# Kernel tuning notes

Hardware: AMD Instinct MI355X
Metric: run time of the kernel (lower is better)

The kernel has to match this reference:

```python
import jax, jax.numpy as jnp
import numpy as np

B, N, T, DM, H, M = 32, 207, 24, 64, 8, 32
E = 2 * DM  # true input feature dim (2*dmodel per the reshape in the source)


def setup_inputs() -> dict:
    rng = jax.random.key(0)
    ks = jax.random.split(rng, 10)
    s = 0.05  # scale params to keep activations numerically sane
    query = jax.random.normal(ks[0], (B, N, T, E), jnp.float32)
    key = jax.random.normal(ks[1], (B, N, T, E), jnp.float32)
    value = jax.random.normal(ks[2], (B, N, T, E), jnp.float32)
    # causal temporal mask, broadcast over batch/node/head; True = masked out
    atten_mask = jnp.broadcast_to(jnp.triu(jnp.ones((T, T), bool), 1), (B, N, 1, T, T))
    qp1 = jax.random.normal(ks[3], (N * DM, M), jnp.float32) * s
    qp2 = jax.random.normal(ks[4], (M, 4 * DM), jnp.float32) * s
    kp1 = jax.random.normal(ks[5], (N * DM, M), jnp.float32) * s
    kp2 = jax.random.normal(ks[6], (M, 4 * DM), jnp.float32) * s
    vp1 = jax.random.normal(ks[7], (N * DM, M), jnp.float32) * s
    vp2 = jax.random.normal(ks[8], (M, 4 * DM), jnp.float32) * s
    out_W = jax.random.normal(ks[9], (E, DM), jnp.float32) * s
    out_b = jnp.zeros((DM,), jnp.float32)
    return dict(query=query, key=key, value=value, atten_mask=atten_mask,
                qp1=qp1, qp2=qp2, kp1=kp1, kp2=kp2, vp1=vp1, vp2=vp2,
                out_W=out_W, out_b=out_b, num_heads=H)


def reference(query, key, value, atten_mask, qp1, qp2, kp1, kp2, vp1, vp2, out_W, out_b, num_heads):
    b, n, t, e = query.shape

    def proj(x, p1, p2):
        # low-rank factored per-node projection: (N*dmodel, M) @ (M, 4*dmodel) -> (N, E, E)
        P = (p1 @ p2).reshape(n, e, e)
        y = jnp.einsum('bnti,nik->bntk', x, P)
        return jax.nn.relu(y).reshape(b, n, t, num_heads, -1)

    q = proj(query, qp1, qp2)   # (B,N,T,H,d)
    k = proj(key, kp1, kp2)
    v = proj(value, vp1, vp2)

    scale = 1.0 / np.sqrt(q.shape[-1]).astype(np.float32)
    scores = jnp.einsum('bnthe,bnshe->bnhts', q, k)          # (B,N,H,T,S)
    scores = jnp.where(atten_mask, -jnp.inf, scores)          # masked_fill before scaling
    attn = jax.nn.softmax(scale * scores, axis=-1)            # dropout disabled (eval)
    out = jnp.einsum('bnhts,bnshd->bnthd', attn, v).reshape(b, n, t, -1)
    out = jax.nn.relu(out @ out_W + out_b)                    # (B,N,T,dmodel)
    return out, attn
```

## Files before the change

### kernel.cpp

```cpp
#include <hip/hip_runtime.h>
#include <hip/hip_bf16.h>

#define Bn 32
#define Nn 207
#define Tt 24
#define Ee 128
#define Hh 8
#define Dm 64
#define Mm 32
#define NBN (Bn * Nn)
#define PT ((size_t)Nn * 16384)

typedef __attribute__((ext_vector_type(8))) short bf16x8;
typedef __attribute__((ext_vector_type(4))) float f32x4;

__device__ __forceinline__ unsigned swz256(unsigned a) { return a ^ (((a >> 8) & 7u) << 4); }
__device__ __forceinline__ unsigned swz64(unsigned a)  { return a ^ (((a >> 7) & 3u) << 4); }
__device__ __forceinline__ unsigned cvtpk(float lo, float hi) {
  unsigned r;
  asm("v_cvt_pk_bf16_f32 %0, %1, %2" : "=v"(r) : "v"(lo), "v"(hi));
  return r;
}
__device__ __forceinline__ unsigned short f2bs(float f) {
  return (unsigned short)cvtpk(f, f);
}

__global__ __launch_bounds__(256) void build_P_frag3(
    const float* __restrict__ qp1, const float* __restrict__ qp2,
    const float* __restrict__ kp1, const float* __restrict__ kp2,
    const float* __restrict__ vp1, const float* __restrict__ vp2,
    unsigned short* __restrict__ Pt) {
  const int tau = blockIdx.y;
  const float* p1 = (tau == 0) ? qp1 : (tau == 1) ? kp1 : vp1;
  const float* p2 = (tau == 0) ? qp2 : (tau == 1) ? kp2 : vp2;
  unsigned short* dst = Pt + (size_t)tau * PT;
  const int bid = blockIdx.x;
  const int n = bid >> 3;
  const int r8 = bid & 7;
  const int ks = r8 >> 1;
  const int chunk = ((r8 & 1) << 1) + (threadIdx.x >> 7);
  const int col = threadIdx.x & 127;
  const int base_i = ks * 32 + chunk * 8;
  const float* p1r = p1 + (size_t)(n * 64 + (base_i >> 1)) * Mm;
  const float* p2a = p2 + col;
  const float* p2b = p2 + 128 + col;
  float acc[8] = {};
#pragma unroll
  for (int m = 0; m < Mm; ++m) {
    float a = p2a[m * 256], b = p2b[m * 256];
#pragma unroll
    for (int jj = 0; jj < 4; ++jj) {
      float pv = p1r[jj * Mm + m];
      acc[2 * jj]     = fmaf(pv, a, acc[2 * jj]);
      acc[2 * jj + 1] = fmaf(pv, b, acc[2 * jj + 1]);
    }
  }
  const int nt = col >> 4;
  const int lane = (chunk << 4) | (col & 15);
  union { unsigned u[4]; uint4 v; } w;
#pragma unroll
  for (int jj = 0; jj < 4; ++jj) w.u[jj] = cvtpk(acc[2 * jj], acc[2 * jj + 1]);
  *(uint4*)(dst + (size_t)(((n * 8 + nt) * 4 + ks) * 64 + lane) * 8) = w.v;
}

__global__ __launch_bounds__(256) void build_W_frag(const float* __restrict__ W,
                                                    unsigned short* __restrict__ Wt) {
  for (int idx = threadIdx.x; idx < 1024; idx += 256) {
    int lane = idx & 63, ks = (idx >> 6) & 3, nt = idx >> 8;
    union { unsigned u[4]; uint4 v; } w;
#pragma unroll
    for (int jj = 0; jj < 4; ++jj) {
      float a = W[(size_t)(ks * 32 + (lane >> 4) * 8 + 2 * jj) * 64 + nt * 16 + (lane & 15)];
      float b = W[(size_t)(ks * 32 + (lane >> 4) * 8 + 2 * jj + 1) * 64 + nt * 16 + (lane & 15)];
      w.u[jj] = cvtpk(a, b);
    }
    *(uint4*)(Wt + (size_t)idx * 8) = w.v;
  }
}

__global__ __launch_bounds__(256, 4) void fused_attn(
    const float* __restrict__ Qin, const float* __restrict__ Kin,
    const float* __restrict__ Vin,
    const unsigned short* __restrict__ Ptq, const unsigned short* __restrict__ Ptk,
    const unsigned short* __restrict__ Ptv, const unsigned short* __restrict__ Wt,
    const float* __restrict__ bias,
    float* __restrict__ out, float* __restrict__ attn) {
  __shared__ __align__(16) char smem[38912];
  const int tid = threadIdx.x;
  const int lane = tid & 63;
  const int wv = tid >> 6;
  const int c = lane & 15;
  const int g = lane >> 4;
  const f32x4 zf = {0.f, 0.f, 0.f, 0.f};
  const bf16x8 zb = {0, 0, 0, 0, 0, 0, 0, 0};

  int bx = blockIdx.x;
  bx = (bx & 7) * 828 + (bx >> 3);
  const int n = bx >> 5;
  const int b = bx & 31;
  const size_t xbase = (size_t)(b * Nn + n) * (Tt * Ee);

  {
    uint4 z4 = {0, 0, 0, 0};
    *(uint4*)(smem + 30720 + tid * 32) = z4;
    *(uint4*)(smem + 30720 + tid * 32 + 16) = z4;
    const float* src[3] = {Qin + xbase, Kin + xbase, Vin + xbase};
#pragma unroll
    for (int w = 0; w < 3; ++w)
#pragma unroll
      for (int it = 0; it < 3; ++it) {
        int e4 = tid + 256 * it;
        float4 xv = *(const float4*)(src[w] + (size_t)e4 * 4);
        unsigned a = swz256((unsigned)((e4 >> 5) * 256 + (e4 & 31) * 8));
        uint2 pk;
        pk.x = cvtpk(xv.x, xv.y);
        pk.y = cvtpk(xv.z, xv.w);
        *(uint2*)(smem + w * 6144 + a) = pk;
      }
  }
  __syncthreads();

  {
#pragma unroll
    for (int w = 0; w < 3; ++w) {
      const unsigned short* Pf = (w == 0) ? Ptq : (w == 1) ? Ptk : Ptv;
      f32x4 acc[2][2] = {{zf, zf}, {zf, zf}};
#pragma unroll
      for (int ks = 0; ks < 4; ++ks) {
        bf16x8 Bf[2], Af[2];
#pragma unroll
        for (int ntl = 0; ntl < 2; ++ntl)
          Bf[ntl] = *(const bf16x8*)(Pf + (size_t)(((n * 8 + (wv * 2 + ntl)) * 4 + ks) * 64 + lane) * 8);
#pragma unroll
        for (int mt = 0; mt < 2; ++mt) {
          int row = mt * 16 + c; row = row < 24 ? row : 23;
          Af[mt] = *(const bf16x8*)(smem + w * 6144 + swz256((unsigned)(row * 256 + ks * 64 + g * 16)));
        }
        __builtin_amdgcn_s_setprio(1);
#pragma unroll
        for (int mt = 0; mt < 2; ++mt)
#pragma unroll
          for (int ntl = 0; ntl < 2; ++ntl)
            acc[mt][ntl] = __builtin_amdgcn_mfma_f32_16x16x32_bf16(Af[mt], Bf[ntl], acc[mt][ntl], 0, 0, 0);
        __builtin_amdgcn_s_setprio(0);
      }
      if (w < 2) {
        const float postscale = (w == 0) ? 0.25f : 1.0f;
        char* dst = smem + 18432 + w * 6144;
#pragma unroll
        for (int mt = 0; mt < 2; ++mt)
#pragma unroll
          for (int r = 0; r < 4; ++r) {
            int row = mt * 16 + g * 4 + r;
            if (row < 24) {
#pragma unroll
              for (int ntl = 0; ntl < 2; ++ntl) {
                int col = (wv * 2 + ntl) * 16 + c;
                *(unsigned short*)(dst + swz256((unsigned)(row * 256 + col * 2))) =
                    f2bs(fmaxf(acc[mt][ntl][r], 0.f) * postscale);
              }
            }
          }
      } else {
#pragma unroll
        for (int mt = 0; mt < 2; ++mt)
#pragma unroll
          for (int r = 0; r < 4; ++r) {
            int srow = mt * 16 + g * 4 + r;
            if (srow < 24) {
#pragma unroll
              for (int ntl = 0; ntl < 2; ++ntl) {
                int dcol = (wv * 2 + ntl) * 16 + c;
                *(unsigned short*)(smem + 30720 + swz64((unsigned)(dcol * 64 + srow * 2))) =
                    f2bs(fmaxf(acc[mt][ntl][r], 0.f));
              }
            }
          }
      }
    }
  }
  __syncthreads();

  {
    const size_t abase = (size_t)(b * Nn + n) * (Hh * Tt * Tt);
#pragma unroll
    for (int hh = 0; hh < 2; ++hh) {
      int h = wv * 2 + hh;
      bf16x8 Aq[2], Bk[2];
#pragma unroll
      for (int mt = 0; mt < 2; ++mt) {
        int row = mt * 16 + c; row = row < 24 ? row : 23;
        Aq[mt] = zb;
        if (lane < 32) Aq[mt] = *(const bf16x8*)(smem + 18432 + swz256((unsigned)(row * 256 + (h * 16 + g * 8) * 2)));
      }
#pragma unroll
      for (int st = 0; st < 2; ++st) {
        int row = st * 16 + c; row = row < 24 ? row : 23;
        Bk[st] = zb;
        if (lane < 32) Bk[st] = *(const bf16x8*)(smem + 24576 + swz256((unsigned)(row * 256 + (h * 16 + g * 8) * 2)));
      }
      f32x4 sc[2][2];
      __builtin_amdgcn_s_setprio(1);
#pragma unroll
      for (int mt = 0; mt < 2; ++mt)
#pragma unroll
        for (int st = 0; st < 2; ++st)
          sc[mt][st] = __builtin_amdgcn_mfma_f32_16x16x32_bf16(Aq[mt], Bk[st], zf, 0, 0, 0);
      __builtin_amdgcn_s_setprio(0);
#pragma unroll
      for (int mt = 0; mt < 2; ++mt)
#pragma unroll
        for (int r = 0; r < 4; ++r) {
          int t = mt * 16 + g * 4 + r;
          float e0 = (c <= t)      ? __expf(sc[mt][0][r]) : 0.f;
          float e1 = (16 + c <= t) ? __expf(sc[mt][1][r]) : 0.f;
          float s2 = e0 + e1;
          s2 += __shfl_xor(s2, 1);
          s2 += __shfl_xor(s2, 2);
          s2 += __shfl_xor(s2, 4);
          s2 += __shfl_xor(s2, 8);
          float inv = 1.0f / s2;
          float p0 = e0 * inv, p1 = e1 * inv;
          if (t < 24) {
            float* ap = attn + abase + (size_t)h * (Tt * Tt) + t * Tt;
            ap[c] = p0;
            if (c < 8) ap[16 + c] = p1;
            *(unsigned short*)(smem + swz64((unsigned)(h * 1536 + t * 64 + c * 2)))        = f2bs(p0);
            *(unsigned short*)(smem + swz64((unsigned)(h * 1536 + t * 64 + (16 + c) * 2))) = f2bs(p1);
          }
        }
    }
  }
  __syncthreads();

  {
    f32x4 pv[2][2];
#pragma unroll
    for (int hh = 0; hh < 2; ++hh) {
      int h = wv * 2 + hh;
      bf16x8 Bv = *(const bf16x8*)(smem + 30720 + swz64((unsigned)((h * 16 + c) * 64 + g * 16)));
#pragma unroll
      for (int mt = 0; mt < 2; ++mt) {
        int row = mt * 16 + c; row = row < 24 ? row : 23;
        bf16x8 Ap = *(const bf16x8*)(smem + swz64((unsigned)(h * 1536 + row * 64 + g * 16)));
        pv[hh][mt] = __builtin_amdgcn_mfma_f32_16x16x32_bf16(Ap, Bv, zf, 0, 0, 0);
      }
    }
#pragma unroll
    for (int hh = 0; hh < 2; ++hh) {
      int h = wv * 2 + hh;
#pragma unroll
      for (int mt = 0; mt < 2; ++mt)
#pragma unroll
        for (int r = 0; r < 4; ++r) {
          int t = mt * 16 + g * 4 + r;
          if (t < 24)
            *(unsigned short*)(smem + 12288 + swz256((unsigned)(t * 256 + (h * 16 + c) * 2))) =
                f2bs(pv[hh][mt][r]);
        }
    }
  }
  __syncthreads();

  {
    f32x4 acc2[2] = {zf, zf};
#pragma unroll
    for (int ks = 0; ks < 4; ++ks) {
      bf16x8 Bw = *(const bf16x8*)(Wt + (size_t)((wv * 4 + ks) * 64 + lane) * 8);
      bf16x8 Af[2];
#pragma unroll
      for (int mt = 0; mt < 2; ++mt) {
        int row = mt * 16 + c; row = row < 24 ? row : 23;
        Af[mt] = *(const bf16x8*)(smem + 12288 + swz256((unsigned)(row * 256 + ks * 64 + g * 16)));
      }
      __builtin_amdgcn_s_setprio(1);
#pragma unroll
      for (int mt = 0; mt < 2; ++mt)
        acc2[mt] = __builtin_amdgcn_mfma_f32_16x16x32_bf16(Af[mt], Bw, acc2[mt], 0, 0, 0);
      __builtin_amdgcn_s_setprio(0);
    }
    int j = wv * 16 + c;
    float bj = bias[j];
    const size_t obase = (size_t)(b * Nn + n) * (Tt * Dm);
#pragma unroll
    for (int mt = 0; mt < 2; ++mt)
#pragma unroll
      for (int r = 0; r < 4; ++r) {
        int t = mt * 16 + g * 4 + r;
        if (t < 24) out[obase + (size_t)t * Dm + j] = fmaxf(acc2[mt][r] + bj, 0.f);
      }
  }
}

extern "C" void kernel_launch(void* const* d_in, const int* in_sizes, int n_in,
                              void* d_out, int out_size, void* d_ws, size_t ws_size,
                              hipStream_t stream) {
  const float* query = (const float*)d_in[0];
  const float* key   = (const float*)d_in[1];
  const float* value = (const float*)d_in[2];
  const float* qp1 = (const float*)d_in[4];
  const float* qp2 = (const float*)d_in[5];
  const float* kp1 = (const float*)d_in[6];
  const float* kp2 = (const float*)d_in[7];
  const float* vp1 = (const float*)d_in[8];
  const float* vp2 = (const float*)d_in[9];
  const float* out_W = (const float*)d_in[10];
  const float* out_b = (const float*)d_in[11];

  unsigned short* Pt  = (unsigned short*)d_ws;
  unsigned short* Wtf = Pt + 3 * PT;

  float* out = (float*)d_out;
  float* attn = out + (size_t)NBN * Tt * Dm;

  build_P_frag3<<<dim3(Nn * 8, 3), 256, 0, stream>>>(qp1, qp2, kp1, kp2, vp1, vp2, Pt);
  build_W_frag<<<1, 256, 0, stream>>>(out_W, Wtf);
  fused_attn<<<NBN, 256, 0, stream>>>(query, key, value,
                                      Pt, Pt + PT, Pt + 2 * PT, Wtf,
                                      out_b, out, attn);
}
```

Before: 169.1 us.

## Project V from registers and write attn via coalesced float4 from LDS

```diff
diff --git a/kernel.cpp b/kernel.cpp
--- a/kernel.cpp
+++ b/kernel.cpp
@@ -23,6 +23,14 @@
 }
 __device__ __forceinline__ unsigned short f2bs(float f) {
   return (unsigned short)cvtpk(f, f);
+}
+__device__ __forceinline__ bf16x8 pack8(float4 a, float4 b) {
+  union { unsigned u[4]; bf16x8 v; } w;
+  w.u[0] = cvtpk(a.x, a.y);
+  w.u[1] = cvtpk(a.z, a.w);
+  w.u[2] = cvtpk(b.x, b.y);
+  w.u[3] = cvtpk(b.z, b.w);
+  return w.v;
 }
 
 __global__ __launch_bounds__(256) void build_P_frag3(
@@ -85,7 +93,7 @@
     const unsigned short* __restrict__ Ptv, const unsigned short* __restrict__ Wt,
     const float* __restrict__ bias,
     float* __restrict__ out, float* __restrict__ attn) {
-  __shared__ __align__(16) char smem[38912];
+  __shared__ __align__(16) char smem[32768];
   const int tid = threadIdx.x;
   const int lane = tid & 63;
   const int wv = tid >> 6;
@@ -102,11 +110,11 @@
 
   {
     uint4 z4 = {0, 0, 0, 0};
-    *(uint4*)(smem + 30720 + tid * 32) = z4;
-    *(uint4*)(smem + 30720 + tid * 32 + 16) = z4;
-    const float* src[3] = {Qin + xbase, Kin + xbase, Vin + xbase};
-#pragma unroll
-    for (int w = 0; w < 3; ++w)
+    *(uint4*)(smem + 24576 + tid * 32) = z4;
+    *(uint4*)(smem + 24576 + tid * 32 + 16) = z4;
+    const float* src[2] = {Qin + xbase, Kin + xbase};
+#pragma unroll
+    for (int w = 0; w < 2; ++w)
 #pragma unroll
       for (int it = 0; it < 3; ++it) {
         int e4 = tid + 256 * it;
@@ -122,8 +130,8 @@
 
   {
 #pragma unroll
-    for (int w = 0; w < 3; ++w) {
-      const unsigned short* Pf = (w == 0) ? Ptq : (w == 1) ? Ptk : Ptv;
+    for (int w = 0; w < 2; ++w) {
+      const unsigned short* Pf = (w == 0) ? Ptq : Ptk;
       f32x4 acc[2][2] = {{zf, zf}, {zf, zf}};
 #pragma unroll
       for (int ks = 0; ks < 4; ++ks) {
@@ -144,45 +152,28 @@
             acc[mt][ntl] = __builtin_amdgcn_mfma_f32_16x16x32_bf16(Af[mt], Bf[ntl], acc[mt][ntl], 0, 0, 0);
         __builtin_amdgcn_s_setprio(0);
       }
-      if (w < 2) {
-        const float postscale = (w == 0) ? 0.25f : 1.0f;
-        char* dst = smem + 18432 + w * 6144;
-#pragma unroll
-        for (int mt = 0; mt < 2; ++mt)
-#pragma unroll
-          for (int r = 0; r < 4; ++r) {
-            int row = mt * 16 + g * 4 + r;
-            if (row < 24) {
-#pragma unroll
-              for (int ntl = 0; ntl < 2; ++ntl) {
-                int col = (wv * 2 + ntl) * 16 + c;
-                *(unsigned short*)(dst + swz256((unsigned)(row * 256 + col * 2))) =
-                    f2bs(fmaxf(acc[mt][ntl][r], 0.f) * postscale);
-              }
+      const float postscale = (w == 0) ? 0.25f : 1.0f;
+      char* dst = smem + 12288 + w * 6144;
+#pragma unroll
+      for (int mt = 0; mt < 2; ++mt)
+#pragma unroll
+        for (int r = 0; r < 4; ++r) {
+          int row = mt * 16 + g * 4 + r;
+          if (row < 24) {
+#pragma unroll
+            for (int ntl = 0; ntl < 2; ++ntl) {
+              int col = (wv * 2 + ntl) * 16 + c;
+              *(unsigned short*)(dst + swz256((unsigned)(row * 256 + col * 2))) =
+                  f2bs(fmaxf(acc[mt][ntl][r], 0.f) * postscale);
             }
           }
-      } else {
-#pragma unroll
-        for (int mt = 0; mt < 2; ++mt)
-#pragma unroll
-          for (int r = 0; r < 4; ++r) {
-            int srow = mt * 16 + g * 4 + r;
-            if (srow < 24) {
-#pragma unroll
-              for (int ntl = 0; ntl < 2; ++ntl) {
-                int dcol = (wv * 2 + ntl) * 16 + c;
-                *(unsigned short*)(smem + 30720 + swz64((unsigned)(dcol * 64 + srow * 2))) =
-                    f2bs(fmaxf(acc[mt][ntl][r], 0.f));
-              }
-            }
-          }
-      }
+        }
     }
   }
   __syncthreads();
 
   {
-    const size_t abase = (size_t)(b * Nn + n) * (Hh * Tt * Tt);
+    f32x4 sc[2][2][2];
 #pragma unroll
     for (int hh = 0; hh < 2; ++hh) {
       int h = wv * 2 + hh;
@@ -191,29 +182,42 @@
       for (int mt = 0; mt < 2; ++mt) {
         int row = mt * 16 + c; row = row < 24 ? row : 23;
         Aq[mt] = zb;
-        if (lane < 32) Aq[mt] = *(const bf16x8*)(smem + 18432 + swz256((unsigned)(row * 256 + (h * 16 + g * 8) * 2)));
+        if (lane < 32) Aq[mt] = *(const bf16x8*)(smem + 12288 + swz256((unsigned)(row * 256 + (h * 16 + g * 8) * 2)));
       }
 #pragma unroll
       for (int st = 0; st < 2; ++st) {
         int row = st * 16 + c; row = row < 24 ? row : 23;
         Bk[st] = zb;
-        if (lane < 32) Bk[st] = *(const bf16x8*)(smem + 24576 + swz256((unsigned)(row * 256 + (h * 16 + g * 8) * 2)));
-      }
-      f32x4 sc[2][2];
+        if (lane < 32) Bk[st] = *(const bf16x8*)(smem + 18432 + swz256((unsigned)(row * 256 + (h * 16 + g * 8) * 2)));
+      }
       __builtin_amdgcn_s_setprio(1);
 #pragma unroll
       for (int mt = 0; mt < 2; ++mt)
 #pragma unroll
         for (int st = 0; st < 2; ++st)
-          sc[mt][st] = __builtin_amdgcn_mfma_f32_16x16x32_bf16(Aq[mt], Bk[st], zf, 0, 0, 0);
+          sc[hh][mt][st] = __builtin_amdgcn_mfma_f32_16x16x32_bf16(Aq[mt], Bk[st], zf, 0, 0, 0);
       __builtin_amdgcn_s_setprio(0);
+    }
+
+    const float* vbase = Vin + xbase;
+    float4 vr[8];
+#pragma unroll
+    for (int ks = 0; ks < 4; ++ks) {
+      const float* p = vbase + (size_t)c * Ee + ks * 32 + g * 8;
+      vr[2 * ks]     = *(const float4*)p;
+      vr[2 * ks + 1] = *(const float4*)(p + 4);
+    }
+
+#pragma unroll
+    for (int hh = 0; hh < 2; ++hh) {
+      int h = wv * 2 + hh;
 #pragma unroll
       for (int mt = 0; mt < 2; ++mt)
 #pragma unroll
         for (int r = 0; r < 4; ++r) {
           int t = mt * 16 + g * 4 + r;
-          float e0 = (c <= t)      ? __expf(sc[mt][0][r]) : 0.f;
-          float e1 = (16 + c <= t) ? __expf(sc[mt][1][r]) : 0.f;
+          float e0 = (c <= t)      ? __expf(sc[hh][mt][0][r]) : 0.f;
+          float e1 = (16 + c <= t) ? __expf(sc[hh][mt][1][r]) : 0.f;
           float s2 = e0 + e1;
           s2 += __shfl_xor(s2, 1);
           s2 += __shfl_xor(s2, 2);
@@ -222,14 +226,57 @@
           float inv = 1.0f / s2;
           float p0 = e0 * inv, p1 = e1 * inv;
           if (t < 24) {
-            float* ap = attn + abase + (size_t)h * (Tt * Tt) + t * Tt;
-            ap[c] = p0;
-            if (c < 8) ap[16 + c] = p1;
             *(unsigned short*)(smem + swz64((unsigned)(h * 1536 + t * 64 + c * 2)))        = f2bs(p0);
             *(unsigned short*)(smem + swz64((unsigned)(h * 1536 + t * 64 + (16 + c) * 2))) = f2bs(p1);
           }
         }
     }
+
+    f32x4 vacc[2][2] = {{zf, zf}, {zf, zf}};
+    {
+      bf16x8 va[4];
+#pragma unroll
+      for (int ks = 0; ks < 4; ++ks) va[ks] = pack8(vr[2 * ks], vr[2 * ks + 1]);
+#pragma unroll
+      for (int ks = 0; ks < 4; ++ks) {
+#pragma unroll
+        for (int ntl = 0; ntl < 2; ++ntl) {
+          bf16x8 Bf = *(const bf16x8*)(Ptv + (size_t)(((n * 8 + (wv * 2 + ntl)) * 4 + ks) * 64 + lane) * 8);
+          vacc[0][ntl] = __builtin_amdgcn_mfma_f32_16x16x32_bf16(va[ks], Bf, vacc[0][ntl], 0, 0, 0);
+        }
+      }
+      int row1 = 16 + c; row1 = row1 < 24 ? row1 : 23;
+#pragma unroll
+      for (int ks = 0; ks < 4; ++ks) {
+        const float* p = vbase + (size_t)row1 * Ee + ks * 32 + g * 8;
+        vr[2 * ks]     = *(const float4*)p;
+        vr[2 * ks + 1] = *(const float4*)(p + 4);
+      }
+#pragma unroll
+      for (int ks = 0; ks < 4; ++ks) va[ks] = pack8(vr[2 * ks], vr[2 * ks + 1]);
+#pragma unroll
+      for (int ks = 0; ks < 4; ++ks) {
+#pragma unroll
+        for (int ntl = 0; ntl < 2; ++ntl) {
+          bf16x8 Bf = *(const bf16x8*)(Ptv + (size_t)(((n * 8 + (wv * 2 + ntl)) * 4 + ks) * 64 + lane) * 8);
+          vacc[1][ntl] = __builtin_amdgcn_mfma_f32_16x16x32_bf16(va[ks], Bf, vacc[1][ntl], 0, 0, 0);
+        }
+      }
+    }
+#pragma unroll
+    for (int mt = 0; mt < 2; ++mt)
+#pragma unroll
+      for (int r = 0; r < 4; ++r) {
+        int srow = mt * 16 + g * 4 + r;
+        if (srow < 24) {
+#pragma unroll
+          for (int ntl = 0; ntl < 2; ++ntl) {
+            int dcol = (wv * 2 + ntl) * 16 + c;
+            *(unsigned short*)(smem + 24576 + swz64((unsigned)(dcol * 64 + srow * 2))) =
+                f2bs(fmaxf(vacc[mt][ntl][r], 0.f));
+          }
+        }
+      }
   }
   __syncthreads();
 
@@ -238,12 +285,30 @@
 #pragma unroll
     for (int hh = 0; hh < 2; ++hh) {
       int h = wv * 2 + hh;
-      bf16x8 Bv = *(const bf16x8*)(smem + 30720 + swz64((unsigned)((h * 16 + c) * 64 + g * 16)));
+      bf16x8 Bv = *(const bf16x8*)(smem + 24576 + swz64((unsigned)((h * 16 + c) * 64 + g * 16)));
 #pragma unroll
       for (int mt = 0; mt < 2; ++mt) {
         int row = mt * 16 + c; row = row < 24 ? row : 23;
         bf16x8 Ap = *(const bf16x8*)(smem + swz64((unsigned)(h * 1536 + row * 64 + g * 16)));
         pv[hh][mt] = __builtin_amdgcn_mfma_f32_16x16x32_bf16(Ap, Bv, zf, 0, 0, 0);
+      }
+    }
+    const size_t abase = (size_t)(b * Nn + n) * (Hh * Tt * Tt);
+#pragma unroll
+    for (int i = 0; i < 5; ++i) {
+      int fidx = tid + 256 * i;
+      if (fidx < 1152) {
+        int h = fidx / 144;
+        int rem = fidx - h * 144;
+        int t = rem / 6;
+        int s4 = (rem - t * 6) * 4;
+        uint2 pr = *(const uint2*)(smem + swz64((unsigned)(h * 1536 + t * 64 + s4 * 2)));
+        float4 o;
+        o.x = __uint_as_float((pr.x & 0xFFFFu) << 16);
+        o.y = __uint_as_float(pr.x & 0xFFFF0000u);
+        o.z = __uint_as_float((pr.y & 0xFFFFu) << 16);
+        o.w = __uint_as_float(pr.y & 0xFFFF0000u);
+        *(float4*)(attn + abase + (size_t)h * 576 + t * 24 + s4) = o;
       }
     }
 #pragma unroll
```

Result: slower. 180.8 us (+6.9%).

## Make attention stages wave-local to drop block barriers and vectorize attn stores

Applied to the files above, without the earlier changes.

```diff
diff --git a/kernel.cpp b/kernel.cpp
--- a/kernel.cpp
+++ b/kernel.cpp
@@ -101,9 +101,11 @@
   const size_t xbase = (size_t)(b * Nn + n) * (Tt * Ee);
 
   {
-    uint4 z4 = {0, 0, 0, 0};
-    *(uint4*)(smem + 30720 + tid * 32) = z4;
-    *(uint4*)(smem + 30720 + tid * 32 + 16) = z4;
+    if (g < 2) {
+      unsigned dcol = (unsigned)(32 * wv + (lane & 31));
+      uint4 z4 = {0, 0, 0, 0};
+      *(uint4*)(smem + 30720 + swz64(dcol * 64 + 48)) = z4;
+    }
     const float* src[3] = {Qin + xbase, Kin + xbase, Vin + xbase};
 #pragma unroll
     for (int w = 0; w < 3; ++w)
@@ -120,143 +122,197 @@
   }
   __syncthreads();
 
+#pragma unroll
+  for (int w = 0; w < 2; ++w) {
+    const unsigned short* Pf = (w == 0) ? Ptq : Ptk;
+    f32x4 acc[2][2] = {{zf, zf}, {zf, zf}};
+#pragma unroll
+    for (int ks = 0; ks < 4; ++ks) {
+      bf16x8 Bf[2], Af[2];
+#pragma unroll
+      for (int ntl = 0; ntl < 2; ++ntl)
+        Bf[ntl] = *(const bf16x8*)(Pf + (size_t)(((n * 8 + (wv * 2 + ntl)) * 4 + ks) * 64 + lane) * 8);
+#pragma unroll
+      for (int mt = 0; mt < 2; ++mt) {
+        int row = mt * 16 + c; row = row < 24 ? row : 23;
+        Af[mt] = *(const bf16x8*)(smem + w * 6144 + swz256((unsigned)(row * 256 + ks * 64 + g * 16)));
+      }
+      __builtin_amdgcn_s_setprio(1);
+#pragma unroll
+      for (int mt = 0; mt < 2; ++mt)
+#pragma unroll
+        for (int ntl = 0; ntl < 2; ++ntl)
+          acc[mt][ntl] = __builtin_amdgcn_mfma_f32_16x16x32_bf16(Af[mt], Bf[ntl], acc[mt][ntl], 0, 0, 0);
+      __builtin_amdgcn_s_setprio(0);
+    }
+    const float postscale = (w == 0) ? 0.25f : 1.0f;
+#pragma unroll
+    for (int mt = 0; mt < 2; ++mt)
+#pragma unroll
+      for (int r = 0; r < 4; ++r) {
+        int row = mt * 16 + g * 4 + r;
+        if (row < 24) {
+#pragma unroll
+          for (int ntl = 0; ntl < 2; ++ntl) {
+            unsigned col2 = (unsigned)((2 * wv + ntl) * 32 + c * 2);
+            unsigned ad = 18432u + w * 6144u + row * 256u + (col2 ^ (((unsigned)row & 3u) << 4));
+            *(unsigned short*)(smem + ad) = f2bs(fmaxf(acc[mt][ntl][r], 0.f) * postscale);
+          }
+        }
+      }
+  }
+
   {
-#pragma unroll
-    for (int w = 0; w < 3; ++w) {
-      const unsigned short* Pf = (w == 0) ? Ptq : (w == 1) ? Ptk : Ptv;
-      f32x4 acc[2][2] = {{zf, zf}, {zf, zf}};
-#pragma unroll
-      for (int ks = 0; ks < 4; ++ks) {
-        bf16x8 Bf[2], Af[2];
+    f32x4 acc[2][2] = {{zf, zf}, {zf, zf}};
+#pragma unroll
+    for (int ks = 0; ks < 4; ++ks) {
+      bf16x8 Bf[2], Af[2];
+#pragma unroll
+      for (int ntl = 0; ntl < 2; ++ntl)
+        Bf[ntl] = *(const bf16x8*)(Ptv + (size_t)(((n * 8 + (wv * 2 + ntl)) * 4 + ks) * 64 + lane) * 8);
+#pragma unroll
+      for (int mt = 0; mt < 2; ++mt) {
+        int row = mt * 16 + c; row = row < 24 ? row : 23;
+        Af[mt] = *(const bf16x8*)(smem + 12288 + swz256((unsigned)(row * 256 + ks * 64 + g * 16)));
+      }
+      __builtin_amdgcn_s_setprio(1);
+#pragma unroll
+      for (int mt = 0; mt < 2; ++mt)
 #pragma unroll
         for (int ntl = 0; ntl < 2; ++ntl)
-          Bf[ntl] = *(const bf16x8*)(Pf + (size_t)(((n * 8 + (wv * 2 + ntl)) * 4 + ks) * 64 + lane) * 8);
-#pragma unroll
-        for (int mt = 0; mt < 2; ++mt) {
-          int row = mt * 16 + c; row = row < 24 ? row : 23;
-          Af[mt] = *(const bf16x8*)(smem + w * 6144 + swz256((unsigned)(row * 256 + ks * 64 + g * 16)));
+          acc[mt][ntl] = __builtin_amdgcn_mfma_f32_16x16x32_bf16(Af[mt], Bf[ntl], acc[mt][ntl], 0, 0, 0);
+      __builtin_amdgcn_s_setprio(0);
+    }
+#pragma unroll
+    for (int mt = 0; mt < 2; ++mt)
+#pragma unroll
+      for (int r = 0; r < 4; ++r) {
+        int srow = mt * 16 + g * 4 + r;
+        if (srow < 24) {
+#pragma unroll
+          for (int ntl = 0; ntl < 2; ++ntl) {
+            int dcol = (wv * 2 + ntl) * 16 + c;
+            *(unsigned short*)(smem + 30720 + swz64((unsigned)(dcol * 64 + srow * 2))) =
+                f2bs(fmaxf(acc[mt][ntl][r], 0.f));
+          }
         }
-        __builtin_amdgcn_s_setprio(1);
-#pragma unroll
-        for (int mt = 0; mt < 2; ++mt)
-#pragma unroll
-          for (int ntl = 0; ntl < 2; ++ntl)
-            acc[mt][ntl] = __builtin_amdgcn_mfma_f32_16x16x32_bf16(Af[mt], Bf[ntl], acc[mt][ntl], 0, 0, 0);
-        __builtin_amdgcn_s_setprio(0);
-      }
-      if (w < 2) {
-        const float postscale = (w == 0) ? 0.25f : 1.0f;
-        char* dst = smem + 18432 + w * 6144;
-#pragma unroll
-        for (int mt = 0; mt < 2; ++mt)
-#pragma unroll
-          for (int r = 0; r < 4; ++r) {
-            int row = mt * 16 + g * 4 + r;
-            if (row < 24) {
-#pragma unroll
-              for (int ntl = 0; ntl < 2; ++ntl) {
-                int col = (wv * 2 + ntl) * 16 + c;
-                *(unsigned short*)(dst + swz256((unsigned)(row * 256 + col * 2))) =
-                    f2bs(fmaxf(acc[mt][ntl][r], 0.f) * postscale);
-              }
-            }
-          }
-      } else {
-#pragma unroll
-        for (int mt = 0; mt < 2; ++mt)
-#pragma unroll
-          for (int r = 0; r < 4; ++r) {
-            int srow = mt * 16 + g * 4 + r;
-            if (srow < 24) {
-#pragma unroll
-              for (int ntl = 0; ntl < 2; ++ntl) {
-                int dcol = (wv * 2 + ntl) * 16 + c;
-                *(unsigned short*)(smem + 30720 + swz64((unsigned)(dcol * 64 + srow * 2))) =
-                    f2bs(fmaxf(acc[mt][ntl][r], 0.f));
-              }
-            }
-          }
-      }
-    }
-  }
-  __syncthreads();
+      }
+  }
+
+  f32x4 sc[2][2][2];
+#pragma unroll
+  for (int hh = 0; hh < 2; ++hh) {
+    int h = wv * 2 + hh;
+    bf16x8 Aq[2], Bk[2];
+#pragma unroll
+    for (int mt = 0; mt < 2; ++mt) {
+      int row = mt * 16 + c; row = row < 24 ? row : 23;
+      Aq[mt] = zb;
+      if (lane < 32) {
+        unsigned col2 = (unsigned)(h * 32 + g * 16);
+        Aq[mt] = *(const bf16x8*)(smem + 18432u + row * 256u + (col2 ^ (((unsigned)row & 3u) << 4)));
+      }
+    }
+#pragma unroll
+    for (int st = 0; st < 2; ++st) {
+      int row = st * 16 + c; row = row < 24 ? row : 23;
+      Bk[st] = zb;
+      if (lane < 32) {
+        unsigned col2 = (unsigned)(h * 32 + g * 16);
+        Bk[st] = *(const bf16x8*)(smem + 24576u + row * 256u + (col2 ^ (((unsigned)row & 3u) << 4)));
+      }
+    }
+    __builtin_amdgcn_s_setprio(1);
+#pragma unroll
+    for (int mt = 0; mt < 2; ++mt)
+#pragma unroll
+      for (int st = 0; st < 2; ++st)
+        sc[hh][mt][st] = __builtin_amdgcn_mfma_f32_16x16x32_bf16(Aq[mt], Bk[st], zf, 0, 0, 0);
+    __builtin_amdgcn_s_setprio(0);
+  }
+
+#pragma unroll
+  for (int hh = 0; hh < 2; ++hh) {
+    int h = wv * 2 + hh;
+    unsigned slot = 18432u + ((unsigned)h & 1u) * 6144u + ((unsigned)h >> 1) * 64u;
+#pragma unroll
+    for (int mt = 0; mt < 2; ++mt)
+#pragma unroll
+      for (int r = 0; r < 4; ++r) {
+        int t = mt * 16 + g * 4 + r;
+        float e0 = (c <= t)      ? __expf(sc[hh][mt][0][r]) : 0.f;
+        float e1 = (16 + c <= t) ? __expf(sc[hh][mt][1][r]) : 0.f;
+        float s2 = e0 + e1;
+        s2 += __shfl_xor(s2, 1);
+        s2 += __shfl_xor(s2, 2);
+        s2 += __shfl_xor(s2, 4);
+        s2 += __shfl_xor(s2, 8);
+        float inv = 1.0f / s2;
+        float p0 = e0 * inv, p1 = e1 * inv;
+        if (t < 24) {
+          unsigned sw = ((unsigned)t & 3u) << 4;
+          *(unsigned short*)(smem + slot + t * 256u + (((unsigned)(c * 2)) ^ sw))      = f2bs(p0);
+          *(unsigned short*)(smem + slot + t * 256u + (((unsigned)(32 + c * 2)) ^ sw)) = f2bs(p1);
+        }
+      }
+  }
 
   {
-    const size_t abase = (size_t)(b * Nn + n) * (Hh * Tt * Tt);
+    bf16x8 Ap[2][2], Bv[2];
 #pragma unroll
     for (int hh = 0; hh < 2; ++hh) {
       int h = wv * 2 + hh;
-      bf16x8 Aq[2], Bk[2];
+      unsigned slot = 18432u + ((unsigned)h & 1u) * 6144u + ((unsigned)h >> 1) * 64u;
+      Bv[hh] = *(const bf16x8*)(smem + 30720 + swz64((unsigned)((h * 16 + c) * 64 + g * 16)));
 #pragma unroll
       for (int mt = 0; mt < 2; ++mt) {
         int row = mt * 16 + c; row = row < 24 ? row : 23;
-        Aq[mt] = zb;
-        if (lane < 32) Aq[mt] = *(const bf16x8*)(smem + 18432 + swz256((unsigned)(row * 256 + (h * 16 + g * 8) * 2)));
-      }
-#pragma unroll
-      for (int st = 0; st < 2; ++st) {
-        int row = st * 16 + c; row = row < 24 ? row : 23;
-        Bk[st] = zb;
-        if (lane < 32) Bk[st] = *(const bf16x8*)(smem + 24576 + swz256((unsigned)(row * 256 + (h * 16 + g * 8) * 2)));
-      }
-      f32x4 sc[2][2];
-      __builtin_amdgcn_s_setprio(1);
-#pragma unroll
-      for (int mt = 0; mt < 2; ++mt)
-#pragma unroll
-        for (int st = 0; st < 2; ++st)
-          sc[mt][st] = __builtin_amdgcn_mfma_f32_16x16x32_bf16(Aq[mt], Bk[st], zf, 0, 0, 0);
-      __builtin_amdgcn_s_setprio(0);
+        Ap[hh][mt] = *(const bf16x8*)(smem + slot + row * 256u +
+                                      (((unsigned)(g * 16)) ^ (((unsigned)row & 3u) << 4)));
+      }
+    }
+    const size_t abase = (size_t)(b * Nn + n) * (Hh * Tt * Tt);
+#pragma unroll
+    for (int i = 0; i < 5; ++i) {
+      int idx = lane + 64 * i;
+      if (idx < 288) {
+        int h_rel = idx / 144;
+        int rem = idx - h_rel * 144;
+        int t = rem / 6;
+        int s4g = rem - t * 6;
+        int h = wv * 2 + h_rel;
+        unsigned slot = 18432u + ((unsigned)h & 1u) * 6144u + ((unsigned)h >> 1) * 64u;
+        uint2 pr = *(const uint2*)(smem + slot + t * 256u +
+                                   (((unsigned)(s4g * 8)) ^ (((unsigned)t & 3u) << 4)));
+        float4 o;
+        o.x = __uint_as_float((pr.x & 0xFFFFu) << 16);
+        o.y = __uint_as_float(pr.x & 0xFFFF0000u);
+        o.z = __uint_as_float((pr.y & 0xFFFFu) << 16);
+        o.w = __uint_as_float(pr.y & 0xFFFF0000u);
+        *(float4*)(attn + abase + (size_t)h * 576 + t * 24 + s4g * 4) = o;
+      }
+    }
+    f32x4 pv[2][2];
+    __builtin_amdgcn_s_setprio(1);
+#pragma unroll
+    for (int hh = 0; hh < 2; ++hh)
+#pragma unroll
+      for (int mt = 0; mt < 2; ++mt)
+        pv[hh][mt] = __builtin_amdgcn_mfma_f32_16x16x32_bf16(Ap[hh][mt], Bv[hh], zf, 0, 0, 0);
+    __builtin_amdgcn_s_setprio(0);
+#pragma unroll
+    for (int hh = 0; hh < 2; ++hh) {
+      int h = wv * 2 + hh;
+      unsigned slot = 18432u + ((unsigned)h & 1u) * 6144u + ((unsigned)h >> 1) * 64u;
 #pragma unroll
       for (int mt = 0; mt < 2; ++mt)
 #pragma unroll
         for (int r = 0; r < 4; ++r) {
           int t = mt * 16 + g * 4 + r;
-          float e0 = (c <= t)      ? __expf(sc[mt][0][r]) : 0.f;
-          float e1 = (16 + c <= t) ? __expf(sc[mt][1][r]) : 0.f;
-          float s2 = e0 + e1;
-          s2 += __shfl_xor(s2, 1);
-          s2 += __shfl_xor(s2, 2);
-          s2 += __shfl_xor(s2, 4);
-          s2 += __shfl_xor(s2, 8);
-          float inv = 1.0f / s2;
-          float p0 = e0 * inv, p1 = e1 * inv;
           if (t < 24) {
-            float* ap = attn + abase + (size_t)h * (Tt * Tt) + t * Tt;
-            ap[c] = p0;
-            if (c < 8) ap[16 + c] = p1;
-            *(unsigned short*)(smem + swz64((unsigned)(h * 1536 + t * 64 + c * 2)))        = f2bs(p0);
-            *(unsigned short*)(smem + swz64((unsigned)(h * 1536 + t * 64 + (16 + c) * 2))) = f2bs(p1);
+            unsigned ad = slot + t * 256u + (((unsigned)(c * 2)) ^ (((unsigned)t & 3u) << 4));
+            *(unsigned short*)(smem + ad) = f2bs(pv[hh][mt][r]);
           }
-        }
-    }
-  }
-  __syncthreads();
-
-  {
-    f32x4 pv[2][2];
-#pragma unroll
-    for (int hh = 0; hh < 2; ++hh) {
-      int h = wv * 2 + hh;
-      bf16x8 Bv = *(const bf16x8*)(smem + 30720 + swz64((unsigned)((h * 16 + c) * 64 + g * 16)));
-#pragma unroll
-      for (int mt = 0; mt < 2; ++mt) {
-        int row = mt * 16 + c; row = row < 24 ? row : 23;
-        bf16x8 Ap = *(const bf16x8*)(smem + swz64((unsigned)(h * 1536 + row * 64 + g * 16)));
-        pv[hh][mt] = __builtin_amdgcn_mfma_f32_16x16x32_bf16(Ap, Bv, zf, 0, 0, 0);
-      }
-    }
-#pragma unroll
-    for (int hh = 0; hh < 2; ++hh) {
-      int h = wv * 2 + hh;
-#pragma unroll
-      for (int mt = 0; mt < 2; ++mt)
-#pragma unroll
-        for (int r = 0; r < 4; ++r) {
-          int t = mt * 16 + g * 4 + r;
-          if (t < 24)
-            *(unsigned short*)(smem + 12288 + swz256((unsigned)(t * 256 + (h * 16 + c) * 2))) =
-                f2bs(pv[hh][mt][r]);
         }
     }
   }
@@ -271,7 +327,9 @@
 #pragma unroll
       for (int mt = 0; mt < 2; ++mt) {
         int row = mt * 16 + c; row = row < 24 ? row : 23;
-        Af[mt] = *(const bf16x8*)(smem + 12288 + swz256((unsigned)(row * 256 + ks * 64 + g * 16)));
+        unsigned ad = 18432u + ((unsigned)(g >> 1)) * 6144u + ((unsigned)ks) * 64u + row * 256u +
+                      ((((unsigned)(g & 1)) * 16u) ^ (((unsigned)row & 3u) << 4));
+        Af[mt] = *(const bf16x8*)(smem + ad);
       }
       __builtin_amdgcn_s_setprio(1);
 #pragma unroll
```

Measured after the change: 163.6 us. -3.2%, faster.

## Keep per-wave heads in private LDS arenas, cut shared memory and barriers

Applied to the files above, without the earlier changes.

```diff
diff --git a/kernel.cpp b/kernel.cpp
--- a/kernel.cpp
+++ b/kernel.cpp
@@ -15,7 +15,6 @@
 typedef __attribute__((ext_vector_type(4))) float f32x4;
 
 __device__ __forceinline__ unsigned swz256(unsigned a) { return a ^ (((a >> 8) & 7u) << 4); }
-__device__ __forceinline__ unsigned swz64(unsigned a)  { return a ^ (((a >> 7) & 3u) << 4); }
 __device__ __forceinline__ unsigned cvtpk(float lo, float hi) {
   unsigned r;
   asm("v_cvt_pk_bf16_f32 %0, %1, %2" : "=v"(r) : "v"(lo), "v"(hi));
@@ -78,14 +77,16 @@
   }
 }
 
-__global__ __launch_bounds__(256, 4) void fused_attn(
+struct P8 { unsigned u[8]; };
+
+__global__ __launch_bounds__(256, 6) void fused_attn(
     const float* __restrict__ Qin, const float* __restrict__ Kin,
     const float* __restrict__ Vin,
     const unsigned short* __restrict__ Ptq, const unsigned short* __restrict__ Ptk,
     const unsigned short* __restrict__ Ptv, const unsigned short* __restrict__ Wt,
     const float* __restrict__ bias,
     float* __restrict__ out, float* __restrict__ attn) {
-  __shared__ __align__(16) char smem[38912];
+  __shared__ __align__(16) char smem[24576];
   const int tid = threadIdx.x;
   const int lane = tid & 63;
   const int wv = tid >> 6;
@@ -101,9 +102,6 @@
   const size_t xbase = (size_t)(b * Nn + n) * (Tt * Ee);
 
   {
-    uint4 z4 = {0, 0, 0, 0};
-    *(uint4*)(smem + 30720 + tid * 32) = z4;
-    *(uint4*)(smem + 30720 + tid * 32 + 16) = z4;
     const float* src[3] = {Qin + xbase, Kin + xbase, Vin + xbase};
 #pragma unroll
     for (int w = 0; w < 3; ++w)
@@ -120,10 +118,12 @@
   }
   __syncthreads();
 
+  P8 pq, pk_, pv_;
   {
 #pragma unroll
     for (int w = 0; w < 3; ++w) {
       const unsigned short* Pf = (w == 0) ? Ptq : (w == 1) ? Ptk : Ptv;
+      const char* xs = smem + w * 6144;
       f32x4 acc[2][2] = {{zf, zf}, {zf, zf}};
 #pragma unroll
       for (int ks = 0; ks < 4; ++ks) {
@@ -134,7 +134,7 @@
 #pragma unroll
         for (int mt = 0; mt < 2; ++mt) {
           int row = mt * 16 + c; row = row < 24 ? row : 23;
-          Af[mt] = *(const bf16x8*)(smem + w * 6144 + swz256((unsigned)(row * 256 + ks * 64 + g * 16)));
+          Af[mt] = *(const bf16x8*)(xs + swz256((unsigned)(row * 256 + ks * 64 + g * 16)));
         }
         __builtin_amdgcn_s_setprio(1);
 #pragma unroll
@@ -144,108 +144,152 @@
             acc[mt][ntl] = __builtin_amdgcn_mfma_f32_16x16x32_bf16(Af[mt], Bf[ntl], acc[mt][ntl], 0, 0, 0);
         __builtin_amdgcn_s_setprio(0);
       }
-      if (w < 2) {
-        const float postscale = (w == 0) ? 0.25f : 1.0f;
-        char* dst = smem + 18432 + w * 6144;
-#pragma unroll
-        for (int mt = 0; mt < 2; ++mt)
-#pragma unroll
-          for (int r = 0; r < 4; ++r) {
-            int row = mt * 16 + g * 4 + r;
-            if (row < 24) {
-#pragma unroll
-              for (int ntl = 0; ntl < 2; ++ntl) {
-                int col = (wv * 2 + ntl) * 16 + c;
-                *(unsigned short*)(dst + swz256((unsigned)(row * 256 + col * 2))) =
-                    f2bs(fmaxf(acc[mt][ntl][r], 0.f) * postscale);
-              }
-            }
+      const float ps = (w == 0) ? 0.25f : 1.0f;
+      P8 r;
+#pragma unroll
+      for (int mt = 0; mt < 2; ++mt)
+#pragma unroll
+        for (int ntl = 0; ntl < 2; ++ntl)
+#pragma unroll
+          for (int half = 0; half < 2; ++half) {
+            float a = fmaxf(acc[mt][ntl][half * 2], 0.f) * ps;
+            float bb = fmaxf(acc[mt][ntl][half * 2 + 1], 0.f) * ps;
+            r.u[(mt * 2 + ntl) * 2 + half] = cvtpk(a, bb);
           }
-      } else {
-#pragma unroll
-        for (int mt = 0; mt < 2; ++mt)
-#pragma unroll
-          for (int r = 0; r < 4; ++r) {
-            int srow = mt * 16 + g * 4 + r;
-            if (srow < 24) {
-#pragma unroll
-              for (int ntl = 0; ntl < 2; ++ntl) {
-                int dcol = (wv * 2 + ntl) * 16 + c;
-                *(unsigned short*)(smem + 30720 + swz64((unsigned)(dcol * 64 + srow * 2))) =
-                    f2bs(fmaxf(acc[mt][ntl][r], 0.f));
-              }
-            }
+      if (w == 0) pq = r; else if (w == 1) pk_ = r; else pv_ = r;
+    }
+  }
+  __syncthreads();
+
+  char* arena = smem + wv * 4608;
+
+#pragma unroll
+  for (int mt = 0; mt < 2; ++mt)
+#pragma unroll
+    for (int ntl = 0; ntl < 2; ++ntl)
+#pragma unroll
+      for (int half = 0; half < 2; ++half) {
+        unsigned uq = pq.u[(mt * 2 + ntl) * 2 + half];
+        unsigned uk = pk_.u[(mt * 2 + ntl) * 2 + half];
+        unsigned uv = pv_.u[(mt * 2 + ntl) * 2 + half];
+#pragma unroll
+        for (int rr = 0; rr < 2; ++rr) {
+          int row = mt * 16 + g * 4 + half * 2 + rr;
+          if (row < 24) {
+            unsigned short vq = (unsigned short)(rr ? (uq >> 16) : uq);
+            unsigned short vk = (unsigned short)(rr ? (uk >> 16) : uk);
+            unsigned short vvv = (unsigned short)(rr ? (uv >> 16) : uv);
+            unsigned adqk = (unsigned)(row * 64) +
+                            (((unsigned)(ntl * 32 + c * 2)) ^ (((unsigned)row & 3u) << 4));
+            *(unsigned short*)(arena + adqk) = vq;
+            *(unsigned short*)(arena + 1536 + adqk) = vk;
+            *(unsigned short*)(arena + 3072 + (ntl * 16 + c) * 48 + row * 2) = vvv;
           }
-      }
-    }
-  }
-  __syncthreads();
+        }
+      }
+
+  bf16x8 Aq[2][2], Bk[2][2];
+#pragma unroll
+  for (int hh = 0; hh < 2; ++hh)
+#pragma unroll
+    for (int mt = 0; mt < 2; ++mt) {
+      int row = mt * 16 + c; row = row < 24 ? row : 23;
+      unsigned ad = (unsigned)(row * 64) +
+                    (((unsigned)(hh * 32 + g * 16)) ^ (((unsigned)row & 3u) << 4));
+      Aq[hh][mt] = zb;
+      Bk[hh][mt] = zb;
+      if (g < 2) {
+        Aq[hh][mt] = *(const bf16x8*)(arena + ad);
+        Bk[hh][mt] = *(const bf16x8*)(arena + 1536 + ad);
+      }
+    }
+
+  unsigned pk0[8];
+#pragma unroll
+  for (int hh = 0; hh < 2; ++hh) {
+    f32x4 sc[2][2];
+    __builtin_amdgcn_s_setprio(1);
+#pragma unroll
+    for (int mt = 0; mt < 2; ++mt)
+#pragma unroll
+      for (int st = 0; st < 2; ++st)
+        sc[mt][st] = __builtin_amdgcn_mfma_f32_16x16x32_bf16(Aq[hh][mt], Bk[hh][st], zf, 0, 0, 0);
+    __builtin_amdgcn_s_setprio(0);
+#pragma unroll
+    for (int mt = 0; mt < 2; ++mt)
+#pragma unroll
+      for (int r = 0; r < 4; ++r) {
+        int t = mt * 16 + g * 4 + r;
+        float e0 = (c <= t)      ? __expf(sc[mt][0][r]) : 0.f;
+        float e1 = (16 + c <= t) ? __expf(sc[mt][1][r]) : 0.f;
+        float s2 = e0 + e1;
+        s2 += __shfl_xor(s2, 1);
+        s2 += __shfl_xor(s2, 2);
+        s2 += __shfl_xor(s2, 4);
+        s2 += __shfl_xor(s2, 8);
+        float inv = 1.0f / s2;
+        float p0 = e0 * inv, p1 = e1 * inv;
+        if (hh == 0) {
+          pk0[mt * 4 + r] = cvtpk(p0, p1);
+        } else {
+          if (t < 24) {
+            *(unsigned short*)(arena + 1152 + t * 48 + c * 2) = f2bs(p0);
+            if (c < 8) *(unsigned short*)(arena + 1152 + t * 48 + (16 + c) * 2) = f2bs(p1);
+          }
+        }
+      }
+  }
+#pragma unroll
+  for (int mt = 0; mt < 2; ++mt)
+#pragma unroll
+    for (int r = 0; r < 4; ++r) {
+      int t = mt * 16 + g * 4 + r;
+      if (t < 24) {
+        unsigned u = pk0[mt * 4 + r];
+        *(unsigned short*)(arena + t * 48 + c * 2) = (unsigned short)u;
+        if (c < 8) *(unsigned short*)(arena + t * 48 + (16 + c) * 2) = (unsigned short)(u >> 16);
+      }
+    }
 
   {
-    const size_t abase = (size_t)(b * Nn + n) * (Hh * Tt * Tt);
+    bf16x8 Ap[2][2], Bv[2];
 #pragma unroll
     for (int hh = 0; hh < 2; ++hh) {
-      int h = wv * 2 + hh;
-      bf16x8 Aq[2], Bk[2];
+      Bv[hh] = zb;
+      if (g < 3) Bv[hh] = *(const bf16x8*)(arena + 3072 + (hh * 16 + c) * 48 + g * 16);
 #pragma unroll
       for (int mt = 0; mt < 2; ++mt) {
         int row = mt * 16 + c; row = row < 24 ? row : 23;
-        Aq[mt] = zb;
-        if (lane < 32) Aq[mt] = *(const bf16x8*)(smem + 18432 + swz256((unsigned)(row * 256 + (h * 16 + g * 8) * 2)));
-      }
-#pragma unroll
-      for (int st = 0; st < 2; ++st) {
-        int row = st * 16 + c; row = row < 24 ? row : 23;
-        Bk[st] = zb;
-        if (lane < 32) Bk[st] = *(const bf16x8*)(smem + 24576 + swz256((unsigned)(row * 256 + (h * 16 + g * 8) * 2)));
-      }
-      f32x4 sc[2][2];
-      __builtin_amdgcn_s_setprio(1);
+        Ap[hh][mt] = zb;
+        if (g < 3) Ap[hh][mt] = *(const bf16x8*)(arena + hh * 1152 + row * 48 + g * 16);
+      }
+    }
+    const size_t abase = (size_t)(b * Nn + n) * (Hh * Tt * Tt);
+#pragma unroll
+    for (int i = 0; i < 5; ++i) {
+      int idx = lane + 64 * i;
+      if (idx < 288) {
+        int hh = idx / 144;
+        int rem = idx - hh * 144;
+        int t = rem / 6;
+        int s4g = rem - t * 6;
+        uint2 pr = *(const uint2*)(arena + hh * 1152 + t * 48 + s4g * 8);
+        float4 o;
+        o.x = __uint_as_float((pr.x & 0xFFFFu) << 16);
+        o.y = __uint_as_float(pr.x & 0xFFFF0000u);
+        o.z = __uint_as_float((pr.y & 0xFFFFu) << 16);
+        o.w = __uint_as_float(pr.y & 0xFFFF0000u);
+        *(float4*)(attn + abase + (size_t)(wv * 2 + hh) * 576 + t * 24 + s4g * 4) = o;
+      }
+    }
+    f32x4 pv[2][2];
+    __builtin_amdgcn_s_setprio(1);
+#pragma unroll
+    for (int hh = 0; hh < 2; ++hh)
 #pragma unroll
       for (int mt = 0; mt < 2; ++mt)
-#pragma unroll
-        for (int st = 0; st < 2; ++st)
-          sc[mt][st] = __builtin_amdgcn_mfma_f32_16x16x32_bf16(Aq[mt], Bk[st], zf, 0, 0, 0);
-      __builtin_amdgcn_s_setprio(0);
-#pragma unroll
-      for (int mt = 0; mt < 2; ++mt)
-#pragma unroll
-        for (int r = 0; r < 4; ++r) {
-          int t = mt * 16 + g * 4 + r;
-          float e0 = (c <= t)      ? __expf(sc[mt][0][r]) : 0.f;
-          float e1 = (16 + c <= t) ? __expf(sc[mt][1][r]) : 0.f;
-          float s2 = e0 + e1;
-          s2 += __shfl_xor(s2, 1);
-          s2 += __shfl_xor(s2, 2);
-          s2 += __shfl_xor(s2, 4);
-          s2 += __shfl_xor(s2, 8);
-          float inv = 1.0f / s2;
-          float p0 = e0 * inv, p1 = e1 * inv;
-          if (t < 24) {
-            float* ap = attn + abase + (size_t)h * (Tt * Tt) + t * Tt;
-            ap[c] = p0;
-            if (c < 8) ap[16 + c] = p1;
-            *(unsigned short*)(smem + swz64((unsigned)(h * 1536 + t * 64 + c * 2)))        = f2bs(p0);
-            *(unsigned short*)(smem + swz64((unsigned)(h * 1536 + t * 64 + (16 + c) * 2))) = f2bs(p1);
-          }
-        }
-    }
-  }
-  __syncthreads();
-
-  {
-    f32x4 pv[2][2];
-#pragma unroll
-    for (int hh = 0; hh < 2; ++hh) {
-      int h = wv * 2 + hh;
-      bf16x8 Bv = *(const bf16x8*)(smem + 30720 + swz64((unsigned)((h * 16 + c) * 64 + g * 16)));
-#pragma unroll
-      for (int mt = 0; mt < 2; ++mt) {
-        int row = mt * 16 + c; row = row < 24 ? row : 23;
-        bf16x8 Ap = *(const bf16x8*)(smem + swz64((unsigned)(h * 1536 + row * 64 + g * 16)));
-        pv[hh][mt] = __builtin_amdgcn_mfma_f32_16x16x32_bf16(Ap, Bv, zf, 0, 0, 0);
-      }
-    }
+        pv[hh][mt] = __builtin_amdgcn_mfma_f32_16x16x32_bf16(Ap[hh][mt], Bv[hh], zf, 0, 0, 0);
+    __builtin_amdgcn_s_setprio(0);
 #pragma unroll
     for (int hh = 0; hh < 2; ++hh) {
       int h = wv * 2 + hh;
@@ -255,28 +299,32 @@
         for (int r = 0; r < 4; ++r) {
           int t = mt * 16 + g * 4 + r;
           if (t < 24)
-            *(unsigned short*)(smem + 12288 + swz256((unsigned)(t * 256 + (h * 16 + c) * 2))) =
+            *(unsigned short*)(smem + 18432 + swz256((unsigned)(t * 256 + (h * 16 + c) * 2))) =
                 f2bs(pv[hh][mt][r]);
         }
     }
   }
+
+  bf16x8 Bw[4];
+#pragma unroll
+  for (int ks = 0; ks < 4; ++ks)
+    Bw[ks] = *(const bf16x8*)(Wt + (size_t)((wv * 4 + ks) * 64 + lane) * 8);
   __syncthreads();
 
   {
     f32x4 acc2[2] = {zf, zf};
 #pragma unroll
     for (int ks = 0; ks < 4; ++ks) {
-      bf16x8 Bw = *(const bf16x8*)(Wt + (size_t)((wv * 4 + ks) * 64 + lane) * 8);
       bf16x8 Af[2];
 #pragma unroll
       for (int mt = 0; mt < 2; ++mt) {
         int row = mt * 16 + c; row = row < 24 ? row : 23;
-        Af[mt] = *(const bf16x8*)(smem + 12288 + swz256((unsigned)(row * 256 + ks * 64 + g * 16)));
+        Af[mt] = *(const bf16x8*)(smem + 18432 + swz256((unsigned)(row * 256 + ks * 64 + g * 16)));
       }
       __builtin_amdgcn_s_setprio(1);
 #pragma unroll
       for (int mt = 0; mt < 2; ++mt)
-        acc2[mt] = __builtin_amdgcn_mfma_f32_16x16x32_bf16(Af[mt], Bw, acc2[mt], 0, 0, 0);
+        acc2[mt] = __builtin_amdgcn_mfma_f32_16x16x32_bf16(Af[mt], Bw[ks], acc2[mt], 0, 0, 0);
       __builtin_amdgcn_s_setprio(0);
     }
     int j = wv * 16 + c;
```

New measurement: 161.0 us. 4.7% less time.
